# Optimization experiments

Hardware: AMD Instinct MI355X
Metric: run time of the kernel (lower is better)

The kernel has to match this reference:

```python
import jax, jax.numpy as jnp
import numpy as np

B, N, D, K = 1024, 8192, 256, 8
LAMBDA_MULT = 0.01

def setup_inputs() -> dict:
    key = jax.random.key(0)
    k1, k2, k3, k4, k5 = jax.random.split(key, 5)
    x = jax.random.uniform(k1, (B, D), dtype=jnp.float32)
    mu = jax.random.uniform(k2, (N, D), dtype=jnp.float32)
    lambda_base = jax.random.uniform(k3, (N,), dtype=jnp.float32) * LAMBDA_MULT
    v = jax.random.normal(k4, (N, K, D), dtype=jnp.float32)  # stands in for per-unit orthogonal init
    omega = 0.1 + 0.4 * jax.random.uniform(k5, (N, K), dtype=jnp.float32)
    return {"x": x, "mu": mu, "lambda_base": lambda_base, "v": v, "omega": omega}

def reference(x, mu, lambda_base, v, omega):
    # quad_form = diff^T (lambda*I + sum_k omega_k v_k v_k^T) diff
    #           = lambda * ||x - mu||^2 + sum_k omega_k * ((x - mu) . v_k)^2
    # Woodbury-style expansion avoids materializing W:(n,d,d) and diff:(b,n,d).
    x2 = jnp.sum(x * x, axis=-1)                      # (b,)
    mu2 = jnp.sum(mu * mu, axis=-1)                   # (n,)
    xm = x @ mu.T                                     # (b,n)
    sqdist = x2[:, None] - 2.0 * xm + mu2[None, :]    # (b,n) = ||x-mu||^2
    xv = jnp.einsum('bd,nkd->bnk', x, v)              # (b,n,k)
    muv = jnp.einsum('nd,nkd->nk', mu, v)             # (n,k)
    proj2 = (xv - muv[None, :, :]) ** 2               # (b,n,k)
    quad = lambda_base[None, :] * sqdist + jnp.einsum('bnk,nk->bn', proj2, omega)
    return jnp.exp(-quad / D)  # Type == 'exp'
```

## Files before the change

kernel.cpp:

```cpp
#include <hip/hip_runtime.h>


#define B_SZ 1024
#define N_SZ 8192
#define D_SZ 256
#define K_SZ 8

#define BTM 256
#define BT 128
#define NT 16

typedef __bf16 bf16x8 __attribute__((ext_vector_type(8)));
typedef float f32x4 __attribute__((ext_vector_type(4)));
typedef unsigned short u16x4 __attribute__((ext_vector_type(4)));
typedef unsigned short u16x8 __attribute__((ext_vector_type(8)));

#define WS_X2   0u
#define WS_MU2  4096u
#define WS_MUV  36864u
#define WS_PX   299008u
#define WS_PW   823296u
#define WS_NEED (823296ull + 37748736ull)

__device__ __forceinline__ float wave_reduce(float s) {
#pragma unroll
  for (int off = 32; off > 0; off >>= 1) s += __shfl_down(s, off);
  return s;
}

__device__ __forceinline__ u16x4 cvt4(float4 t) {
  u16x4 r;
  r[0] = __builtin_bit_cast(unsigned short, (__bf16)t.x);
  r[1] = __builtin_bit_cast(unsigned short, (__bf16)t.y);
  r[2] = __builtin_bit_cast(unsigned short, (__bf16)t.z);
  r[3] = __builtin_bit_cast(unsigned short, (__bf16)t.w);
  return r;
}

__device__ __forceinline__ void glds16(const void* g, const void* l) {
  __builtin_amdgcn_global_load_lds(
      (const __attribute__((address_space(1))) void*)g,
      (__attribute__((address_space(3))) void*)l, 16, 0, 0);
}

__global__ void prep_all(const float* __restrict__ x, const float* __restrict__ mu,
                         const float* __restrict__ v,
                         float* __restrict__ x2, unsigned short* __restrict__ px,
                         float* __restrict__ mu2, float* __restrict__ muv,
                         unsigned short* __restrict__ pw) {
  const int w = threadIdx.x >> 6, lane = threadIdx.x & 63;
  const int g = blockIdx.x * 4 + w;
  if (g < B_SZ) {
    const int b = g;
    float4 t = *(const float4*)(x + (size_t)b * D_SZ + 4 * lane);
    *(u16x4*)(px + (size_t)b * D_SZ + 4 * lane) = cvt4(t);
    float s = t.x * t.x + t.y * t.y + t.z * t.z + t.w * t.w;
    s = wave_reduce(s);
    if (lane == 0) x2[b] = s;
  } else if (g < B_SZ + N_SZ) {
    const int n = g - B_SZ;
    float4 m4 = *(const float4*)(mu + (size_t)n * D_SZ + 4 * lane);
    *(u16x4*)(pw + (size_t)n * 9 * D_SZ + 4 * lane) = cvt4(m4);
    float s = m4.x * m4.x + m4.y * m4.y + m4.z * m4.z + m4.w * m4.w;
    s = wave_reduce(s);
    if (lane == 0) mu2[n] = s;
  } else {
    const int idx = g - (B_SZ + N_SZ);
    const int n = idx >> 3, k = idx & 7;
    float4 m4 = *(const float4*)(mu + (size_t)n * D_SZ + 4 * lane);
    float4 v4 = *(const float4*)(v + ((size_t)n * K_SZ + k) * D_SZ + 4 * lane);
    *(u16x4*)(pw + ((size_t)n * 9 + k + 1) * D_SZ + 4 * lane) = cvt4(v4);
    float s = m4.x * v4.x + m4.y * v4.y + m4.z * v4.z + m4.w * v4.w;
    s = wave_reduce(s);
    if (lane == 0) muv[n * K_SZ + k] = s;
  }
}

__global__ __launch_bounds__(256, 2)
void hmu_main_p(const unsigned short* __restrict__ px,
                const unsigned short* __restrict__ pw,
                const float* __restrict__ lam, const float* __restrict__ om,
                const float* __restrict__ wsf, float* __restrict__ out) {
  __shared__ __align__(16) unsigned short Bs[8 * 144 * 32];

  const float* ws_x2 = wsf;
  const float* ws_mu2 = wsf + 1024;
  const float* ws_muv = wsf + 9216;

  const int tid = threadIdx.x;
  const int lane = tid & 63;
  const int w = tid >> 6;
  const int m = lane & 15;
  const int kg = lane >> 4;

  const int bid = blockIdx.x;
  const int xcd = bid & 7;
  const int idx = bid >> 3;
  const int n0 = (xcd * 64 + (idx >> 2)) * NT;
  const int b0 = (idx & 3) * BTM;

  const unsigned short* pxw = px + (size_t)(b0 + w * 64 + m) * D_SZ + kg * 8;
  bf16x8 a_nxt0 = *(const bf16x8*)(pxw + 0 * 16 * D_SZ);
  bf16x8 a_nxt1 = *(const bf16x8*)(pxw + 1 * 16 * D_SZ);
  bf16x8 a_nxt2 = *(const bf16x8*)(pxw + 2 * 16 * D_SZ);
  bf16x8 a_nxt3 = *(const bf16x8*)(pxw + 3 * 16 * D_SZ);

  {
    const int nl4 = lane >> 2;
    const int ch = lane & 3;
    const int kc = (ch ^ ((nl4 >> 1) & 3)) * 8;
#pragma unroll
    for (int p = 0; p < 18; ++p) {
      const int pair = w * 18 + p;
      const int kt = pair / 9, j = pair % 9;
      glds16(pw + ((size_t)(n0 + nl4) * 9 + j) * D_SZ + kt * 32 + kc,
             Bs + (kt * 144 + j * 16) * 32);
    }
  }
  __syncthreads();

  f32x4 acc[4][9];
#pragma unroll
  for (int rb = 0; rb < 4; ++rb)
#pragma unroll
    for (int j = 0; j < 9; ++j) acc[rb][j] = (f32x4){0.f, 0.f, 0.f, 0.f};

  const int sw = (kg ^ ((m >> 1) & 3)) * 8;

#pragma unroll
  for (int kt = 0; kt < 8; ++kt) {
    bf16x8 a0 = a_nxt0, a1 = a_nxt1, a2 = a_nxt2, a3 = a_nxt3;
    if (kt < 7) {
      a_nxt0 = *(const bf16x8*)(pxw + 0 * 16 * D_SZ + (kt + 1) * 32);
      a_nxt1 = *(const bf16x8*)(pxw + 1 * 16 * D_SZ + (kt + 1) * 32);
      a_nxt2 = *(const bf16x8*)(pxw + 2 * 16 * D_SZ + (kt + 1) * 32);
      a_nxt3 = *(const bf16x8*)(pxw + 3 * 16 * D_SZ + (kt + 1) * 32);
    }
#pragma unroll
    for (int j = 0; j < 9; ++j) {
      bf16x8 bfr = *(const bf16x8*)&Bs[(kt * 144 + j * 16 + m) * 32 + sw];
      acc[0][j] = __builtin_amdgcn_mfma_f32_16x16x32_bf16(a0, bfr, acc[0][j], 0, 0, 0);
      acc[1][j] = __builtin_amdgcn_mfma_f32_16x16x32_bf16(a1, bfr, acc[1][j], 0, 0, 0);
      acc[2][j] = __builtin_amdgcn_mfma_f32_16x16x32_bf16(a2, bfr, acc[2][j], 0, 0, 0);
      acc[3][j] = __builtin_amdgcn_mfma_f32_16x16x32_bf16(a3, bfr, acc[3][j], 0, 0, 0);
    }
  }

  const int n = n0 + m;
  const float lam_n = lam[n];
  const float mu2_n = ws_mu2[n];
  float omr[8], muvr[8];
#pragma unroll
  for (int k = 0; k < 8; ++k) {
    omr[k] = om[n * 8 + k];
    muvr[k] = ws_muv[n * 8 + k];
  }
#pragma unroll
  for (int rb = 0; rb < 4; ++rb) {
#pragma unroll
    for (int r = 0; r < 4; ++r) {
      int b = b0 + (w * 4 + rb) * 16 + kg * 4 + r;
      float x2b = ws_x2[b];
      float c0 = acc[rb][0][r];
      float q = lam_n * (x2b - 2.f * c0 + mu2_n);
#pragma unroll
      for (int k = 0; k < 8; ++k) {
        float p = acc[rb][k + 1][r] - muvr[k];
        q = fmaf(omr[k] * p, p, q);
      }
      out[(size_t)b * N_SZ + n] = __expf(q * (-1.0f / 256.0f));
    }
  }
}

__device__ __forceinline__ void cvt16_store(const float* __restrict__ src,
                                            unsigned short* dst) {
  const float4* p4 = (const float4*)src;
  float fv[16];
#pragma unroll
  for (int e = 0; e < 4; ++e) {
    float4 t = p4[e];
    fv[4 * e + 0] = t.x; fv[4 * e + 1] = t.y;
    fv[4 * e + 2] = t.z; fv[4 * e + 3] = t.w;
  }
  u16x8 lo, hi;
#pragma unroll
  for (int e = 0; e < 8; ++e) {
    lo[e] = __builtin_bit_cast(unsigned short, (__bf16)fv[e]);
    hi[e] = __builtin_bit_cast(unsigned short, (__bf16)fv[e + 8]);
  }
  *(u16x8*)dst = lo;
  *(u16x8*)(dst + 8) = hi;
}

#define LDS_STRIDE 40
__global__ __launch_bounds__(256, 2)
void hmu_main_f(const float* __restrict__ x, const float* __restrict__ mu,
                const float* __restrict__ lam, const float* __restrict__ v,
                const float* __restrict__ om, const float* __restrict__ ws,
                float* __restrict__ out) {
  __shared__ __align__(16) unsigned short As[BT * LDS_STRIDE];
  __shared__ __align__(16) unsigned short Bs[NT * 9 * LDS_STRIDE];
  const float* ws_x2 = ws;
  const float* ws_mu2 = ws + 1024;
  const float* ws_muv = ws + 9216;
  const int tid = threadIdx.x, lane = tid & 63, w = tid >> 6;
  const int m = lane & 15, kg = lane >> 4;
  const int n0 = blockIdx.x * NT, b0 = blockIdx.y * BT;
  f32x4 acc[2][9];
#pragma unroll
  for (int bs = 0; bs < 2; ++bs)
#pragma unroll
    for (int j = 0; j < 9; ++j) acc[bs][j] = (f32x4){0.f, 0.f, 0.f, 0.f};
  const int arow = tid >> 1, ahalf = tid & 1;
  for (int kt = 0; kt < 8; ++kt) {
    const int k0 = kt * 32;
    cvt16_store(x + (size_t)(b0 + arow) * D_SZ + k0 + ahalf * 16,
                &As[arow * LDS_STRIDE + ahalf * 16]);
#pragma unroll
    for (int it = 0; it < 2; ++it) {
      int idx = tid + 256 * it;
      if (idx < 288) {
        int row = idx >> 1, half = idx & 1;
        int nl = row / 9, j = row - nl * 9;
        const float* src = (j == 0)
            ? mu + (size_t)(n0 + nl) * D_SZ + k0 + half * 16
            : v + (size_t)((n0 + nl) * K_SZ + (j - 1)) * D_SZ + k0 + half * 16;
        cvt16_store(src, &Bs[row * LDS_STRIDE + half * 16]);
      }
    }
    __syncthreads();
    bf16x8 af[2];
#pragma unroll
    for (int bs = 0; bs < 2; ++bs)
      af[bs] = *(const bf16x8*)&As[((2 * w + bs) * 16 + m) * LDS_STRIDE + kg * 8];
#pragma unroll
    for (int j = 0; j < 9; ++j) {
      bf16x8 bfr = *(const bf16x8*)&Bs[(m * 9 + j) * LDS_STRIDE + kg * 8];
      acc[0][j] = __builtin_amdgcn_mfma_f32_16x16x32_bf16(af[0], bfr, acc[0][j], 0, 0, 0);
      acc[1][j] = __builtin_amdgcn_mfma_f32_16x16x32_bf16(af[1], bfr, acc[1][j], 0, 0, 0);
    }
    __syncthreads();
  }
  const int n = n0 + m;
  const float lam_n = lam[n];
  const float mu2_n = ws_mu2[n];
  float omr[8], muvr[8];
#pragma unroll
  for (int k = 0; k < 8; ++k) {
    omr[k] = om[n * 8 + k];
    muvr[k] = ws_muv[n * 8 + k];
  }
#pragma unroll
  for (int bs = 0; bs < 2; ++bs)
#pragma unroll
    for (int r = 0; r < 4; ++r) {
      int b = b0 + (2 * w + bs) * 16 + kg * 4 + r;
      float c0 = acc[bs][0][r];
      float q = lam_n * (ws_x2[b] - 2.f * c0 + mu2_n);
#pragma unroll
      for (int k = 0; k < 8; ++k) {
        float p = acc[bs][k + 1][r] - muvr[k];
        q = fmaf(omr[k] * p, p, q);
      }
      out[(size_t)b * N_SZ + n] = __expf(q * (-1.0f / 256.0f));
    }
}

__global__ void p2_mu_f(const float* __restrict__ mu, const float* __restrict__ v,
                        float* __restrict__ mu2, float* __restrict__ muv) {
  __shared__ __align__(16) float mulds[D_SZ];
  const int n = blockIdx.x;
  const int w = threadIdx.x >> 6, lane = threadIdx.x & 63;
  if (w == 0) {
    float4 m4 = *(const float4*)(mu + (size_t)n * D_SZ + 4 * lane);
    *(float4*)(mulds + 4 * lane) = m4;
    float s = m4.x * m4.x + m4.y * m4.y + m4.z * m4.z + m4.w * m4.w;
    s = wave_reduce(s);
    if (lane == 0) mu2[n] = s;
  }
  __syncthreads();
  float4 m4 = *(const float4*)(mulds + 4 * lane);
#pragma unroll
  for (int kk = 0; kk < 2; ++kk) {
    const int k = w * 2 + kk;
    float4 v4 = *(const float4*)(v + ((size_t)n * K_SZ + k) * D_SZ + 4 * lane);
    float s = m4.x * v4.x + m4.y * v4.y + m4.z * v4.z + m4.w * v4.w;
    s = wave_reduce(s);
    if (lane == 0) muv[n * K_SZ + k] = s;
  }
}

__global__ void p1_x2_f(const float* __restrict__ x, float* __restrict__ x2) {
  const int w = threadIdx.x >> 6, lane = threadIdx.x & 63;
  const int b = blockIdx.x * 4 + w;
  float4 t = *(const float4*)(x + (size_t)b * D_SZ + 4 * lane);
  float s = t.x * t.x + t.y * t.y + t.z * t.z + t.w * t.w;
  s = wave_reduce(s);
  if (lane == 0) x2[b] = s;
}

extern "C" void kernel_launch(void* const* d_in, const int* in_sizes, int n_in,
                              void* d_out, int out_size, void* d_ws, size_t ws_size,
                              hipStream_t stream) {
  const float* x   = (const float*)d_in[0];
  const float* mu  = (const float*)d_in[1];
  const float* lam = (const float*)d_in[2];
  const float* v   = (const float*)d_in[3];
  const float* om  = (const float*)d_in[4];
  float* out = (float*)d_out;
  char* wsb = (char*)d_ws;
  float* wsf = (float*)d_ws;
  float* x2  = (float*)(wsb + WS_X2);
  float* mu2 = (float*)(wsb + WS_MU2);
  float* muv = (float*)(wsb + WS_MUV);

  if (ws_size >= WS_NEED) {
    unsigned short* px = (unsigned short*)(wsb + WS_PX);
    unsigned short* pw = (unsigned short*)(wsb + WS_PW);
    const int nunits = B_SZ + N_SZ + N_SZ * K_SZ;
    prep_all<<<nunits / 4, 256, 0, stream>>>(x, mu, v, x2, px, mu2, muv, pw);
    hmu_main_p<<<(N_SZ / NT) * (B_SZ / BTM), 256, 0, stream>>>(px, pw, lam, om, wsf, out);
  } else {
    dim3 grid(N_SZ / NT, B_SZ / BT);
    p1_x2_f<<<B_SZ / 4, 256, 0, stream>>>(x, x2);
    p2_mu_f<<<N_SZ, 256, 0, stream>>>(mu, v, mu2, muv);
    hmu_main_f<<<grid, 256, 0, stream>>>(x, mu, lam, v, om, wsf, out);
  }
}
```

Measured before the change: 169.7 us.

## Split B-tile columns across wave pairs and double-buffer A fragments

Halves the batch tile per block (BTM 256→128), so each block covers 128 rows with four waves. Waves are paired: one wave of each pair computes the distance column plus four projections, the other computes the remaining four projections, and partial quadratic sums are combined through shared memory. The A-operand loads now use a two-deep register buffer. This doubles the block count and cuts accumulator registers per wave, aiming at better occupancy and latency hiding. The cost is an extra LDS round-trip and barrier, twice the B-tile loading per output, and uneven MFMA work between the two halves (5 vs 4 columns).

```diff
diff --git a/kernel.cpp b/kernel.cpp
--- a/kernel.cpp
+++ b/kernel.cpp
@@ -6,7 +6,7 @@
 #define D_SZ 256
 #define K_SZ 8
 
-#define BTM 256
+#define BTM 128
 #define BT 128
 #define NT 16
 
@@ -90,20 +90,16 @@
   const int tid = threadIdx.x;
   const int lane = tid & 63;
   const int w = tid >> 6;
+  const int w2 = w & 1;
+  const int jh = w >> 1;
   const int m = lane & 15;
   const int kg = lane >> 4;
 
   const int bid = blockIdx.x;
   const int xcd = bid & 7;
   const int idx = bid >> 3;
-  const int n0 = (xcd * 64 + (idx >> 2)) * NT;
-  const int b0 = (idx & 3) * BTM;
-
-  const unsigned short* pxw = px + (size_t)(b0 + w * 64 + m) * D_SZ + kg * 8;
-  bf16x8 a_nxt0 = *(const bf16x8*)(pxw + 0 * 16 * D_SZ);
-  bf16x8 a_nxt1 = *(const bf16x8*)(pxw + 1 * 16 * D_SZ);
-  bf16x8 a_nxt2 = *(const bf16x8*)(pxw + 2 * 16 * D_SZ);
-  bf16x8 a_nxt3 = *(const bf16x8*)(pxw + 3 * 16 * D_SZ);
+  const int n0 = (xcd * 64 + (idx >> 3)) * NT;
+  const int b0 = (idx & 7) * BTM;
 
   {
     const int nl4 = lane >> 2;
@@ -117,59 +113,99 @@
              Bs + (kt * 144 + j * 16) * 32);
     }
   }
+
+  const unsigned short* pxw = px + (size_t)(b0 + w2 * 64 + m) * D_SZ + kg * 8;
+  bf16x8 abuf[2][4];
+#pragma unroll
+  for (int t = 0; t < 2; ++t)
+#pragma unroll
+    for (int rb = 0; rb < 4; ++rb)
+      abuf[t][rb] = *(const bf16x8*)(pxw + (size_t)rb * 16 * D_SZ + t * 32);
+
   __syncthreads();
 
-  f32x4 acc[4][9];
+  f32x4 acc[4][5];
 #pragma unroll
   for (int rb = 0; rb < 4; ++rb)
 #pragma unroll
-    for (int j = 0; j < 9; ++j) acc[rb][j] = (f32x4){0.f, 0.f, 0.f, 0.f};
+    for (int j = 0; j < 5; ++j) acc[rb][j] = (f32x4){0.f, 0.f, 0.f, 0.f};
 
   const int sw = (kg ^ ((m >> 1) & 3)) * 8;
+  const int jbase = jh * 5;
+  const int jn = 5 - jh;
 
 #pragma unroll
   for (int kt = 0; kt < 8; ++kt) {
-    bf16x8 a0 = a_nxt0, a1 = a_nxt1, a2 = a_nxt2, a3 = a_nxt3;
-    if (kt < 7) {
-      a_nxt0 = *(const bf16x8*)(pxw + 0 * 16 * D_SZ + (kt + 1) * 32);
-      a_nxt1 = *(const bf16x8*)(pxw + 1 * 16 * D_SZ + (kt + 1) * 32);
-      a_nxt2 = *(const bf16x8*)(pxw + 2 * 16 * D_SZ + (kt + 1) * 32);
-      a_nxt3 = *(const bf16x8*)(pxw + 3 * 16 * D_SZ + (kt + 1) * 32);
-    }
-#pragma unroll
-    for (int j = 0; j < 9; ++j) {
-      bf16x8 bfr = *(const bf16x8*)&Bs[(kt * 144 + j * 16 + m) * 32 + sw];
-      acc[0][j] = __builtin_amdgcn_mfma_f32_16x16x32_bf16(a0, bfr, acc[0][j], 0, 0, 0);
-      acc[1][j] = __builtin_amdgcn_mfma_f32_16x16x32_bf16(a1, bfr, acc[1][j], 0, 0, 0);
-      acc[2][j] = __builtin_amdgcn_mfma_f32_16x16x32_bf16(a2, bfr, acc[2][j], 0, 0, 0);
-      acc[3][j] = __builtin_amdgcn_mfma_f32_16x16x32_bf16(a3, bfr, acc[3][j], 0, 0, 0);
+    const int sl = kt & 1;
+#pragma unroll
+    for (int j = 0; j < 5; ++j) {
+      if (j < jn) {
+        bf16x8 bfr =
+            *(const bf16x8*)&Bs[(kt * 144 + (jbase + j) * 16 + m) * 32 + sw];
+        acc[0][j] = __builtin_amdgcn_mfma_f32_16x16x32_bf16(abuf[sl][0], bfr, acc[0][j], 0, 0, 0);
+        acc[1][j] = __builtin_amdgcn_mfma_f32_16x16x32_bf16(abuf[sl][1], bfr, acc[1][j], 0, 0, 0);
+        acc[2][j] = __builtin_amdgcn_mfma_f32_16x16x32_bf16(abuf[sl][2], bfr, acc[2][j], 0, 0, 0);
+        acc[3][j] = __builtin_amdgcn_mfma_f32_16x16x32_bf16(abuf[sl][3], bfr, acc[3][j], 0, 0, 0);
+      }
+    }
+    if (kt < 6) {
+#pragma unroll
+      for (int rb = 0; rb < 4; ++rb)
+        abuf[sl][rb] =
+            *(const bf16x8*)(pxw + (size_t)rb * 16 * D_SZ + (kt + 2) * 32);
     }
   }
 
   const int n = n0 + m;
-  const float lam_n = lam[n];
-  const float mu2_n = ws_mu2[n];
-  float omr[8], muvr[8];
-#pragma unroll
-  for (int k = 0; k < 8; ++k) {
-    omr[k] = om[n * 8 + k];
-    muvr[k] = ws_muv[n * 8 + k];
-  }
-#pragma unroll
-  for (int rb = 0; rb < 4; ++rb) {
-#pragma unroll
-    for (int r = 0; r < 4; ++r) {
-      int b = b0 + (w * 4 + rb) * 16 + kg * 4 + r;
-      float x2b = ws_x2[b];
-      float c0 = acc[rb][0][r];
-      float q = lam_n * (x2b - 2.f * c0 + mu2_n);
-#pragma unroll
-      for (int k = 0; k < 8; ++k) {
-        float p = acc[rb][k + 1][r] - muvr[k];
-        q = fmaf(omr[k] * p, p, q);
-      }
-      out[(size_t)b * N_SZ + n] = __expf(q * (-1.0f / 256.0f));
-    }
+  __syncthreads();
+  float(*sL)[17] = (float(*)[17])Bs;
+
+  if (jh == 1) {
+    float omr[4], muvr[4];
+#pragma unroll
+    for (int k = 0; k < 4; ++k) {
+      omr[k] = om[n * 8 + 4 + k];
+      muvr[k] = ws_muv[n * 8 + 4 + k];
+    }
+#pragma unroll
+    for (int rb = 0; rb < 4; ++rb)
+#pragma unroll
+      for (int r = 0; r < 4; ++r) {
+        int row = w2 * 64 + rb * 16 + kg * 4 + r;
+        float s = 0.f;
+#pragma unroll
+        for (int k = 0; k < 4; ++k) {
+          float p = acc[rb][k][r] - muvr[k];
+          s = fmaf(omr[k] * p, p, s);
+        }
+        sL[row][m] = s;
+      }
+  }
+  __syncthreads();
+  if (jh == 0) {
+    const float lam_n = lam[n];
+    const float mu2_n = ws_mu2[n];
+    float omr[4], muvr[4];
+#pragma unroll
+    for (int k = 0; k < 4; ++k) {
+      omr[k] = om[n * 8 + k];
+      muvr[k] = ws_muv[n * 8 + k];
+    }
+#pragma unroll
+    for (int rb = 0; rb < 4; ++rb)
+#pragma unroll
+      for (int r = 0; r < 4; ++r) {
+        int row = w2 * 64 + rb * 16 + kg * 4 + r;
+        int b = b0 + row;
+        float c0 = acc[rb][0][r];
+        float q = lam_n * (ws_x2[b] - 2.f * c0 + mu2_n) + sL[row][m];
+#pragma unroll
+        for (int k = 0; k < 4; ++k) {
+          float p = acc[rb][k + 1][r] - muvr[k];
+          q = fmaf(omr[k] * p, p, q);
+        }
+        out[(size_t)b * N_SZ + n] = __expf(q * (-1.0f / 256.0f));
+      }
   }
 }
 
```

After: 204.9 us. +20.7%, slower.
